# Kernel optimization log

Measured on AMD Instinct MI355X. Metric: run time of the kernel, lower is better.

The kernel has to match this reference:

```python
import jax, jax.numpy as jnp
import numpy as np

MODES = 256


def setup_inputs() -> dict:
    key = jax.random.key(0)
    k1, k2, k3, k4, k5 = jax.random.split(key, 5)
    B, C_IN, C_OUT, N, KM = 8, 128, 128, 8192, 32
    scale = 1.0 / (C_IN * C_OUT)
    return {
        "x": jax.random.normal(k1, (B, C_IN, N), dtype=jnp.float32),
        "wbases": jax.random.normal(k2, (B, N, MODES), dtype=jnp.float32),
        "bases": jax.random.normal(k3, (B, N, MODES), dtype=jnp.float32),
        "weights": scale * jax.random.normal(k4, (C_IN, C_OUT, KM), dtype=jnp.float32),
        "D": jax.random.normal(k5, (KM, MODES), dtype=jnp.float32),
    }


def reference(x, wbases, bases, weights, D):
    # Project onto weighted bases: (b, c_in, n) x (b, n, modes) -> (b, c_in, modes)
    x_hat = jnp.einsum('bcx,bxk->bck', x, wbases[:, :, :MODES])
    # D-weighted channel mixing. Original: x_hat1[b,i,j,k] = x_hat[b,i,k]*D[j,k];
    # y[b,o,k] = sum_{i,j} x_hat1[b,i,j,k] * weights[i,o,j]
    # Equivalent fused contraction (same math, no 4D broadcast):
    y_hat = jnp.einsum('bik,jk,ioj->bok', x_hat, D, weights)
    # Reconstruct on output bases: (b, c_out, modes) x (b, n, modes) -> (b, c_out, n)
    y = jnp.einsum('bck,bxk->bcx', y_hat, bases[:, :, :MODES])
    return y
```

## Files before the change

kernel.cpp:

```cpp
#include <hip/hip_runtime.h>

#define B_    8
#define CIN   128
#define COUT  128
#define NX    8192
#define KMJ   32
#define MODES 256

typedef short bf16x8 __attribute__((ext_vector_type(8)));
typedef float f32x4  __attribute__((ext_vector_type(4)));

__device__ __forceinline__ float bf2f(unsigned short u) {
    union { unsigned int i; float f; } v; v.i = ((unsigned int)u) << 16; return v.f;
}
__device__ __forceinline__ unsigned short f2bf(float f) {
    union { float f; unsigned int i; } v; v.f = f;
    unsigned int x = v.i;
    return (unsigned short)((x + 0x7fffu + ((x >> 16) & 1u)) >> 16);
}
__device__ __forceinline__ bf16x8 cvt8(const float* __restrict__ p) {
    f32x4 a = *(const f32x4*)p;
    f32x4 b = *(const f32x4*)(p + 4);
    bf16x8 r;
    r[0] = (short)f2bf(a[0]); r[1] = (short)f2bf(a[1]);
    r[2] = (short)f2bf(a[2]); r[3] = (short)f2bf(a[3]);
    r[4] = (short)f2bf(b[0]); r[5] = (short)f2bf(b[1]);
    r[6] = (short)f2bf(b[2]); r[7] = (short)f2bf(b[3]);
    return r;
}
__device__ __forceinline__ ushort4 cvt4(f32x4 a) {
    ushort4 r;
    r.x = f2bf(a[0]); r.y = f2bf(a[1]); r.z = f2bf(a[2]); r.w = f2bf(a[3]);
    return r;
}

__global__ __launch_bounds__(256) void k1_wk(const float* __restrict__ W,
                                             const float* __restrict__ D,
                                             unsigned short* __restrict__ Wk) {
    int wave = threadIdx.x >> 6, lane = threadIdx.x & 63;
    int quad = lane >> 4, l16 = lane & 15;
    int gw  = blockIdx.x * 4 + wave;
    int oi0 = gw * 16;
    int i0  = oi0 & 127, o0 = oi0 >> 7;
    bf16x8 bfrag = cvt8(W + ((size_t)(i0 + l16) * COUT + o0) * KMJ + quad * 8);
#pragma unroll
    for (int m = 0; m < 4; m++) {
        int k0 = (blockIdx.y * 4 + m) * 16;
        bf16x8 afrag;
#pragma unroll
        for (int jj = 0; jj < 8; jj++)
            afrag[jj] = (short)f2bf(D[(quad * 8 + jj) * MODES + k0 + l16]);
        f32x4 acc = {0.f, 0.f, 0.f, 0.f};
        acc = __builtin_amdgcn_mfma_f32_16x16x32_bf16(afrag, bfrag, acc, 0, 0, 0);
#pragma unroll
        for (int r = 0; r < 4; r++)
            Wk[(size_t)(k0 + quad * 4 + r) * (CIN * COUT) + oi0 + l16] = f2bf(acc[r]);
    }
}

__global__ __launch_bounds__(1024, 4) void k2_xhat(const float* __restrict__ X,
                                                   const float* __restrict__ WB,
                                                   unsigned short* __restrict__ PART) {
    __shared__ __align__(16) unsigned short Xs[128 * 40];
    __shared__ __align__(16) unsigned short WBT[256 * 40];
    int nt = blockIdx.x, b = blockIdx.y;
    int r0 = nt * 256;
    int t  = threadIdx.x;
    int wave = t >> 6, lane = t & 63;
    int wm = wave >> 2, wk = wave & 3;
    int quad = lane >> 4, l16 = lane & 15;
    int sw = quad ^ (l16 & 3);

    const float* xb  = X  + (size_t)b * CIN * NX;
    const float* wbb = WB + (size_t)b * NX * MODES;

    bool isX = (t >= 512);
    int j  = t & 511;
    int xr = j >> 2, xseg = j & 3;
    int kseg = j >> 4, np2 = j & 15;

    const float* gx = xb + (size_t)xr * NX + r0 + xseg * 8;
    const float* gw = wbb + (size_t)(r0 + 2 * np2) * MODES + 8 * kseg;
    unsigned short* xw = Xs + xr * 40 + ((xseg ^ (xr & 3)) << 3);

    f32x4 acc[2][4];
#pragma unroll
    for (int i = 0; i < 2; i++)
#pragma unroll
        for (int jj = 0; jj < 4; jj++) acc[i][jj] = (f32x4){0.f, 0.f, 0.f, 0.f};

    f32x4 st0, st1, st2, st3;
    if (isX) {
        st0 = *(const f32x4*)gx; st1 = *(const f32x4*)(gx + 4);
    } else {
        st0 = *(const f32x4*)gw;           st1 = *(const f32x4*)(gw + 4);
        st2 = *(const f32x4*)(gw + MODES); st3 = *(const f32x4*)(gw + MODES + 4);
    }

    for (int p = 0; p < 8; p++) {
        if (p) __syncthreads();
        if (isX) {
            *(ushort4*)xw       = cvt4(st0);
            *(ushort4*)(xw + 4) = cvt4(st1);
        } else {
#pragma unroll
            for (int jj = 0; jj < 8; jj++) {
                int k = 8 * kseg + jj;
                float v0 = (jj < 4) ? st0[jj] : st1[jj - 4];
                float v1 = (jj < 4) ? st2[jj] : st3[jj - 4];
                unsigned int w = (unsigned int)f2bf(v0) |
                                 ((unsigned int)f2bf(v1) << 16);
                *(unsigned int*)(WBT + k * 40 + (((np2 >> 2) ^ (k & 3)) << 3) + ((np2 & 3) << 1)) = w;
            }
        }
        __syncthreads();

        if (p < 7) {
            if (isX) {
                gx += 32;
                st0 = *(const f32x4*)gx; st1 = *(const f32x4*)(gx + 4);
            } else {
                gw += (size_t)32 * MODES;
                st0 = *(const f32x4*)gw;           st1 = *(const f32x4*)(gw + 4);
                st2 = *(const f32x4*)(gw + MODES); st3 = *(const f32x4*)(gw + MODES + 4);
            }
        }

        bf16x8 af[2], bfv[4];
#pragma unroll
        for (int tm = 0; tm < 2; tm++)
            af[tm] = *(const bf16x8*)(Xs + (wm * 32 + tm * 16 + l16) * 40 + (sw << 3));
#pragma unroll
        for (int tn = 0; tn < 4; tn++)
            bfv[tn] = *(const bf16x8*)(WBT + (wk * 64 + tn * 16 + l16) * 40 + (sw << 3));
#pragma unroll
        for (int tm = 0; tm < 2; tm++)
#pragma unroll
            for (int tn = 0; tn < 4; tn++)
                acc[tm][tn] = __builtin_amdgcn_mfma_f32_16x16x32_bf16(af[tm], bfv[tn], acc[tm][tn], 0, 0, 0);
    }

    unsigned short* pb = PART + ((size_t)b * 32 + nt) * (CIN * MODES);
#pragma unroll
    for (int tm = 0; tm < 2; tm++) {
        int c = wm * 32 + tm * 16 + quad * 4;
#pragma unroll
        for (int tn = 0; tn < 4; tn++) {
            int km = wk * 64 + tn * 16 + l16;
#pragma unroll
            for (int r = 0; r < 4; r++)
                pb[(size_t)(c + r) * MODES + km] = f2bf(acc[tm][tn][r]);
        }
    }
}

__global__ __launch_bounds__(256) void k2b_red(const unsigned short* __restrict__ PART,
                                               float* __restrict__ XH) {
    int e = blockIdx.x * 256 + threadIdx.x;
    const unsigned short* p = PART + (size_t)(e >> 15) * 32 * (CIN * MODES) + (e & 32767);
    float acc = 0.f;
#pragma unroll
    for (int nt = 0; nt < 32; nt++) acc += bf2f(p[nt * (CIN * MODES)]);
    XH[e] = acc;
}

__global__ __launch_bounds__(256, 2) void k3_yhat(const float* __restrict__ XH,
                                                  const unsigned short* __restrict__ Wk,
                                                  unsigned short* __restrict__ YH) {
    __shared__ float xs[128][8];
    int k = blockIdx.x, oh = blockIdx.y;
    int t = threadIdx.x;
#pragma unroll
    for (int l = 0; l < 4; l++) {
        int e = l * 256 + t;
        int i = e >> 3, bb = e & 7;
        xs[i][bb] = XH[(size_t)bb * (CIN * MODES) + (size_t)i * MODES + k];
    }
    int o = oh * 64 + (t & 63), bq = t >> 6;
    const unsigned short* wp = Wk + (size_t)k * (CIN * COUT) + (size_t)o * CIN;
    bf16x8 wc[16];
#pragma unroll
    for (int ii = 0; ii < 16; ii++)
        wc[ii] = *(const bf16x8*)(wp + ii * 8);
    __syncthreads();
    float a0 = 0.f, a1 = 0.f;
#pragma unroll
    for (int ii = 0; ii < 16; ii++)
#pragma unroll
        for (int jj = 0; jj < 8; jj++) {
            float w = bf2f((unsigned short)wc[ii][jj]);
            int i = ii * 8 + jj;
            a0 += w * xs[i][bq * 2];
            a1 += w * xs[i][bq * 2 + 1];
        }
    YH[((size_t)(bq * 2)     * COUT + o) * MODES + k] = f2bf(a0);
    YH[((size_t)(bq * 2 + 1) * COUT + o) * MODES + k] = f2bf(a1);
}

__global__ __launch_bounds__(1024, 8) void k4_y(const unsigned short* __restrict__ YH,
                                                const float* __restrict__ BA,
                                                float* __restrict__ Y) {
    __shared__ __align__(16) unsigned short As[128 * 40];
    __shared__ __align__(16) unsigned short Bs[128 * 40];
    int b  = blockIdx.y;
    int n0 = blockIdx.x * 128;
    int t  = threadIdx.x;
    int wave = t >> 6, lane = t & 63;
    int wm = wave >> 2, wn = wave & 3;
    int quad = lane >> 4, l16 = lane & 15;
    int sw = quad ^ (l16 & 3);

    const unsigned short* yhb = YH + (size_t)b * COUT * MODES;
    const float* bab = BA + (size_t)b * NX * MODES + (size_t)n0 * MODES;

    bool isA = (t < 512);
    int j  = t & 511;
    int rr = j >> 2, seg = j & 3;
    int ssw = (seg ^ (rr & 3)) << 3;

    const unsigned short* ga = yhb + (size_t)rr * MODES + seg * 8;
    const float* gb = bab + (size_t)rr * MODES + seg * 8;

    f32x4 acc[2][2];
#pragma unroll
    for (int i = 0; i < 2; i++)
#pragma unroll
        for (int jj = 0; jj < 2; jj++) acc[i][jj] = (f32x4){0.f, 0.f, 0.f, 0.f};

    bf16x8 sa; f32x4 sb0, sb1;
    if (isA) sa = *(const bf16x8*)ga;
    else { sb0 = *(const f32x4*)gb; sb1 = *(const f32x4*)(gb + 4); }

    for (int p = 0; p < 8; p++) {
        if (p) __syncthreads();
        if (isA) {
            *(bf16x8*)(As + rr * 40 + ssw) = sa;
        } else {
            bf16x8 v;
            v[0] = (short)f2bf(sb0[0]); v[1] = (short)f2bf(sb0[1]);
            v[2] = (short)f2bf(sb0[2]); v[3] = (short)f2bf(sb0[3]);
            v[4] = (short)f2bf(sb1[0]); v[5] = (short)f2bf(sb1[1]);
            v[6] = (short)f2bf(sb1[2]); v[7] = (short)f2bf(sb1[3]);
            *(bf16x8*)(Bs + rr * 40 + ssw) = v;
        }
        __syncthreads();

        if (p < 7) {
            if (isA) { ga += 32; sa = *(const bf16x8*)ga; }
            else     { gb += 32; sb0 = *(const f32x4*)gb; sb1 = *(const f32x4*)(gb + 4); }
        }

        bf16x8 af[2], bfv[2];
#pragma unroll
        for (int tm = 0; tm < 2; tm++)
            af[tm] = *(const bf16x8*)(As + (wm * 32 + tm * 16 + l16) * 40 + (sw << 3));
#pragma unroll
        for (int tn = 0; tn < 2; tn++)
            bfv[tn] = *(const bf16x8*)(Bs + (wn * 32 + tn * 16 + l16) * 40 + (sw << 3));
#pragma unroll
        for (int tm = 0; tm < 2; tm++)
#pragma unroll
            for (int tn = 0; tn < 2; tn++)
                acc[tm][tn] = __builtin_amdgcn_mfma_f32_16x16x32_bf16(af[tm], bfv[tn], acc[tm][tn], 0, 0, 0);
    }

    float* yb = Y + (size_t)b * COUT * NX;
#pragma unroll
    for (int tm = 0; tm < 2; tm++) {
        int o = wm * 32 + tm * 16 + quad * 4;
#pragma unroll
        for (int tn = 0; tn < 2; tn++) {
            int n = n0 + wn * 32 + tn * 16 + l16;
#pragma unroll
            for (int r = 0; r < 4; r++)
                yb[(size_t)(o + r) * NX + n] = acc[tm][tn][r];
        }
    }
}

extern "C" void kernel_launch(void* const* d_in, const int* in_sizes, int n_in,
                              void* d_out, int out_size, void* d_ws, size_t ws_size,
                              hipStream_t stream) {
    const float* X  = (const float*)d_in[0];
    const float* WB = (const float*)d_in[1];
    const float* BA = (const float*)d_in[2];
    const float* W  = (const float*)d_in[3];
    const float* D  = (const float*)d_in[4];
    float* Y = (float*)d_out;

    char* ws = (char*)d_ws;
    unsigned short* Wk   = (unsigned short*)ws;
    float*          XH   = (float*)(ws + (8u << 20));
    unsigned short* YH   = (unsigned short*)(ws + (9u << 20));
    unsigned short* PART = (unsigned short*)(ws + (10u << 20));

    k1_wk  <<<dim3(256, 4),   256,  0, stream>>>(W, D, Wk);
    k2_xhat<<<dim3(32, 8),    1024, 0, stream>>>(X, WB, PART);
    k2b_red<<<1024,           256,  0, stream>>>(PART, XH);
    k3_yhat<<<dim3(256, 2),   256,  0, stream>>>(XH, Wk, YH);
    k4_y   <<<dim3(64, 8),    1024, 0, stream>>>(YH, BA, Y);
}
```

Before: 220.4 us.

## Load MFMA fragments directly from global memory, dropping LDS staging in k2 and k4

Removes the shared-memory staging tiles and the barriers from both big GEMM kernels. Each wave now reads its MFMA A/B fragments straight from global memory and converts them to bf16 in registers. This saves LDS traffic and synchronisation, but each block re-reads operands that waves used to share, which adds redundant global/L2 traffic. In k2 the wbases load becomes a strided gather of scalar floats, one per row at MODES stride.

```diff
diff --git a/kernel.cpp b/kernel.cpp
--- a/kernel.cpp
+++ b/kernel.cpp
@@ -28,11 +28,6 @@
     r[6] = (short)f2bf(b[2]); r[7] = (short)f2bf(b[3]);
     return r;
 }
-__device__ __forceinline__ ushort4 cvt4(f32x4 a) {
-    ushort4 r;
-    r.x = f2bf(a[0]); r.y = f2bf(a[1]); r.z = f2bf(a[2]); r.w = f2bf(a[3]);
-    return r;
-}
 
 __global__ __launch_bounds__(256) void k1_wk(const float* __restrict__ W,
                                              const float* __restrict__ D,
@@ -58,30 +53,22 @@
     }
 }
 
-__global__ __launch_bounds__(1024, 4) void k2_xhat(const float* __restrict__ X,
-                                                   const float* __restrict__ WB,
-                                                   unsigned short* __restrict__ PART) {
-    __shared__ __align__(16) unsigned short Xs[128 * 40];
-    __shared__ __align__(16) unsigned short WBT[256 * 40];
+__global__ __launch_bounds__(1024) void k2_xhat(const float* __restrict__ X,
+                                                const float* __restrict__ WB,
+                                                unsigned short* __restrict__ PART) {
     int nt = blockIdx.x, b = blockIdx.y;
     int r0 = nt * 256;
     int t  = threadIdx.x;
     int wave = t >> 6, lane = t & 63;
     int wm = wave >> 2, wk = wave & 3;
     int quad = lane >> 4, l16 = lane & 15;
-    int sw = quad ^ (l16 & 3);
 
     const float* xb  = X  + (size_t)b * CIN * NX;
     const float* wbb = WB + (size_t)b * NX * MODES;
 
-    bool isX = (t >= 512);
-    int j  = t & 511;
-    int xr = j >> 2, xseg = j & 3;
-    int kseg = j >> 4, np2 = j & 15;
-
-    const float* gx = xb + (size_t)xr * NX + r0 + xseg * 8;
-    const float* gw = wbb + (size_t)(r0 + 2 * np2) * MODES + 8 * kseg;
-    unsigned short* xw = Xs + xr * 40 + ((xseg ^ (xr & 3)) << 3);
+    const float* xr0 = xb + (size_t)(wm * 32 + l16) * NX + r0 + quad * 8;
+    const float* xr1 = xr0 + (size_t)16 * NX;
+    const float* wc0 = wbb + (size_t)(r0 + quad * 8) * MODES + wk * 64 + l16;
 
     f32x4 acc[2][4];
 #pragma unroll
@@ -89,50 +76,19 @@
 #pragma unroll
         for (int jj = 0; jj < 4; jj++) acc[i][jj] = (f32x4){0.f, 0.f, 0.f, 0.f};
 
-    f32x4 st0, st1, st2, st3;
-    if (isX) {
-        st0 = *(const f32x4*)gx; st1 = *(const f32x4*)(gx + 4);
-    } else {
-        st0 = *(const f32x4*)gw;           st1 = *(const f32x4*)(gw + 4);
-        st2 = *(const f32x4*)(gw + MODES); st3 = *(const f32x4*)(gw + MODES + 4);
-    }
-
+#pragma unroll 2
     for (int p = 0; p < 8; p++) {
-        if (p) __syncthreads();
-        if (isX) {
-            *(ushort4*)xw       = cvt4(st0);
-            *(ushort4*)(xw + 4) = cvt4(st1);
-        } else {
-#pragma unroll
-            for (int jj = 0; jj < 8; jj++) {
-                int k = 8 * kseg + jj;
-                float v0 = (jj < 4) ? st0[jj] : st1[jj - 4];
-                float v1 = (jj < 4) ? st2[jj] : st3[jj - 4];
-                unsigned int w = (unsigned int)f2bf(v0) |
-                                 ((unsigned int)f2bf(v1) << 16);
-                *(unsigned int*)(WBT + k * 40 + (((np2 >> 2) ^ (k & 3)) << 3) + ((np2 & 3) << 1)) = w;
-            }
-        }
-        __syncthreads();
-
-        if (p < 7) {
-            if (isX) {
-                gx += 32;
-                st0 = *(const f32x4*)gx; st1 = *(const f32x4*)(gx + 4);
-            } else {
-                gw += (size_t)32 * MODES;
-                st0 = *(const f32x4*)gw;           st1 = *(const f32x4*)(gw + 4);
-                st2 = *(const f32x4*)(gw + MODES); st3 = *(const f32x4*)(gw + MODES + 4);
-            }
-        }
-
-        bf16x8 af[2], bfv[4];
-#pragma unroll
-        for (int tm = 0; tm < 2; tm++)
-            af[tm] = *(const bf16x8*)(Xs + (wm * 32 + tm * 16 + l16) * 40 + (sw << 3));
-#pragma unroll
-        for (int tn = 0; tn < 4; tn++)
-            bfv[tn] = *(const bf16x8*)(WBT + (wk * 64 + tn * 16 + l16) * 40 + (sw << 3));
+        bf16x8 af[2];
+        af[0] = cvt8(xr0 + p * 32);
+        af[1] = cvt8(xr1 + p * 32);
+        bf16x8 bfv[4];
+#pragma unroll
+        for (int tn = 0; tn < 4; tn++) {
+            const float* wp = wc0 + (size_t)p * 32 * MODES + tn * 16;
+#pragma unroll
+            for (int jj = 0; jj < 8; jj++)
+                bfv[tn][jj] = (short)f2bf(wp[(size_t)jj * MODES]);
+        }
 #pragma unroll
         for (int tm = 0; tm < 2; tm++)
 #pragma unroll
@@ -197,29 +153,23 @@
     YH[((size_t)(bq * 2 + 1) * COUT + o) * MODES + k] = f2bf(a1);
 }
 
-__global__ __launch_bounds__(1024, 8) void k4_y(const unsigned short* __restrict__ YH,
-                                                const float* __restrict__ BA,
-                                                float* __restrict__ Y) {
-    __shared__ __align__(16) unsigned short As[128 * 40];
-    __shared__ __align__(16) unsigned short Bs[128 * 40];
+__global__ __launch_bounds__(1024) void k4_y(const unsigned short* __restrict__ YH,
+                                             const float* __restrict__ BA,
+                                             float* __restrict__ Y) {
     int b  = blockIdx.y;
     int n0 = blockIdx.x * 128;
     int t  = threadIdx.x;
     int wave = t >> 6, lane = t & 63;
     int wm = wave >> 2, wn = wave & 3;
     int quad = lane >> 4, l16 = lane & 15;
-    int sw = quad ^ (l16 & 3);
 
     const unsigned short* yhb = YH + (size_t)b * COUT * MODES;
     const float* bab = BA + (size_t)b * NX * MODES + (size_t)n0 * MODES;
 
-    bool isA = (t < 512);
-    int j  = t & 511;
-    int rr = j >> 2, seg = j & 3;
-    int ssw = (seg ^ (rr & 3)) << 3;
-
-    const unsigned short* ga = yhb + (size_t)rr * MODES + seg * 8;
-    const float* gb = bab + (size_t)rr * MODES + seg * 8;
+    const unsigned short* ya0 = yhb + (size_t)(wm * 32 + l16) * MODES + quad * 8;
+    const unsigned short* ya1 = ya0 + (size_t)16 * MODES;
+    const float* bb0 = bab + (size_t)(wn * 32 + l16) * MODES + quad * 8;
+    const float* bb1 = bb0 + (size_t)16 * MODES;
 
     f32x4 acc[2][2];
 #pragma unroll
@@ -227,36 +177,13 @@
 #pragma unroll
         for (int jj = 0; jj < 2; jj++) acc[i][jj] = (f32x4){0.f, 0.f, 0.f, 0.f};
 
-    bf16x8 sa; f32x4 sb0, sb1;
-    if (isA) sa = *(const bf16x8*)ga;
-    else { sb0 = *(const f32x4*)gb; sb1 = *(const f32x4*)(gb + 4); }
-
+#pragma unroll 2
     for (int p = 0; p < 8; p++) {
-        if (p) __syncthreads();
-        if (isA) {
-            *(bf16x8*)(As + rr * 40 + ssw) = sa;
-        } else {
-            bf16x8 v;
-            v[0] = (short)f2bf(sb0[0]); v[1] = (short)f2bf(sb0[1]);
-            v[2] = (short)f2bf(sb0[2]); v[3] = (short)f2bf(sb0[3]);
-            v[4] = (short)f2bf(sb1[0]); v[5] = (short)f2bf(sb1[1]);
-            v[6] = (short)f2bf(sb1[2]); v[7] = (short)f2bf(sb1[3]);
-            *(bf16x8*)(Bs + rr * 40 + ssw) = v;
-        }
-        __syncthreads();
-
-        if (p < 7) {
-            if (isA) { ga += 32; sa = *(const bf16x8*)ga; }
-            else     { gb += 32; sb0 = *(const f32x4*)gb; sb1 = *(const f32x4*)(gb + 4); }
-        }
-
         bf16x8 af[2], bfv[2];
-#pragma unroll
-        for (int tm = 0; tm < 2; tm++)
-            af[tm] = *(const bf16x8*)(As + (wm * 32 + tm * 16 + l16) * 40 + (sw << 3));
-#pragma unroll
-        for (int tn = 0; tn < 2; tn++)
-            bfv[tn] = *(const bf16x8*)(Bs + (wn * 32 + tn * 16 + l16) * 40 + (sw << 3));
+        af[0] = *(const bf16x8*)(ya0 + p * 32);
+        af[1] = *(const bf16x8*)(ya1 + p * 32);
+        bfv[0] = cvt8(bb0 + p * 32);
+        bfv[1] = cvt8(bb1 + p * 32);
 #pragma unroll
         for (int tm = 0; tm < 2; tm++)
 #pragma unroll
```

Result: slower. 253.6 us (+15.1%).
